# Kernel optimization log

Hardware: AMD Instinct MI355X
Metric: run time of the kernel (lower is better)

## Reference

```python
import jax, jax.numpy as jnp
import numpy as np

B, K, L, D, H, A = 32, 512, 6, 2048, 16, 10
HD = D // H
OBS = 128
MAX_STEPS = 512


def _ln(x, g, b, eps=1e-5):
    m = x.mean(-1, keepdims=True)
    v = ((x - m) ** 2).mean(-1, keepdims=True)
    return (x - m) * jax.lax.rsqrt(v + eps) * g + b


def _pos_encoding(seq_len, dim):
    # torch: seq counts down from seq_len-1 to 0
    seq = jnp.arange(seq_len - 1, -1, -1, dtype=jnp.float32)
    inv = 10000.0 ** (-(jnp.arange(0, dim, 2, dtype=jnp.float32)) / dim)
    si = seq[:, None] * inv[None, :]
    return jnp.concatenate([jnp.sin(si), jnp.cos(si)], axis=-1)  # [seq_len, dim]


def setup_inputs() -> dict:
    key = jax.random.key(0)
    ks = jax.random.split(key, 16)
    s = 0.02
    inp = {}
    inp['x'] = jax.random.normal(ks[0], (B, OBS), jnp.float32)
    inp['memories'] = jax.random.normal(ks[1], (B, K, L, D), jnp.float32)
    inp['mask'] = jax.random.randint(ks[2], (B, K), 0, 2, jnp.int32)
    inp['memory_indices'] = jax.random.randint(ks[3], (B, K), 0, MAX_STEPS, jnp.int32)
    # encoder (vector-obs Linear)
    inp['enc_w'] = jax.random.normal(ks[4], (D, OBS), jnp.float32) * s
    inp['enc_b'] = jnp.zeros((D,), jnp.float32)
    # per-layer params, stacked on leading L axis
    inp['lnq_g'] = jnp.ones((L, D), jnp.float32)
    inp['lnq_b'] = jnp.zeros((L, D), jnp.float32)
    inp['lnkv_g'] = jnp.ones((L, D), jnp.float32)
    inp['lnkv_b'] = jnp.zeros((L, D), jnp.float32)
    inp['lnattn_g'] = jnp.ones((L, D), jnp.float32)
    inp['lnattn_b'] = jnp.zeros((L, D), jnp.float32)
    inp['wq'] = jax.random.normal(ks[5], (L, HD, HD), jnp.float32) * s
    inp['wk'] = jax.random.normal(ks[6], (L, HD, HD), jnp.float32) * s
    inp['wv'] = jax.random.normal(ks[7], (L, HD, HD), jnp.float32) * s
    inp['wo'] = jax.random.normal(ks[8], (L, D, D), jnp.float32) * s
    inp['bo'] = jnp.zeros((L, D), jnp.float32)
    inp['fc_w'] = jax.random.normal(ks[9], (L, D, D), jnp.float32) * s
    inp['fc_b'] = jnp.zeros((L, D), jnp.float32)
    # heads
    inp['post_w'] = jax.random.normal(ks[10], (D, D), jnp.float32) * s
    inp['post_b'] = jnp.zeros((D,), jnp.float32)
    inp['actor_w'] = jax.random.normal(ks[11], (A, D), jnp.float32) * 0.01
    inp['actor_b'] = jnp.zeros((A,), jnp.float32)
    inp['critic_w'] = jax.random.normal(ks[12], (1, D), jnp.float32) * s
    inp['critic_b'] = jnp.zeros((1,), jnp.float32)
    return inp


def reference(x, memories, mask, memory_indices, enc_w, enc_b,
              lnq_g, lnq_b, lnkv_g, lnkv_b, lnattn_g, lnattn_b,
              wq, wk, wv, wo, bo, fc_w, fc_b,
              post_w, post_b, actor_w, actor_b, critic_w, critic_b):
    h = x @ enc_w.T + enc_b                              # [B, D] encoder
    pe = _pos_encoding(MAX_STEPS, D)[memory_indices]      # [B, K, D]
    mems = memories + pe[:, :, None, :]                   # [B, K, L, D]
    mems_t = jnp.moveaxis(mems, 2, 0)                     # [L, B, K, D]
    maskf = mask[:, None, :] != 0                         # [B, 1, K] -> bcast over heads
    inv_scale = 1.0 / jnp.sqrt(jnp.float32(D))            # note: full embed_dim, as in source

    def body(xq, p):
        lg, lb, kg, kb, ag, ab, Wq, Wk, Wv, Wo, bo_, Fw, Fb, mem = p
        q_ = _ln(xq, lg, lb)                              # [B, D] (query LN)
        kv = _ln(mem, kg, kb)                             # [B, K, D] (key = value = LN(mem))
        q = jnp.einsum('bhd,ed->bhe', q_.reshape(B, H, HD), Wq)
        k = jnp.einsum('bkhd,ed->bkhe', kv.reshape(B, K, H, HD), Wk)
        v = jnp.einsum('bkhd,ed->bkhe', kv.reshape(B, K, H, HD), Wv)
        energy = jnp.einsum('bhd,bkhd->bhk', q, k)        # [B, H, K]
        energy = jnp.where(maskf, energy, jnp.float32(-1e20))
        attn = jax.nn.softmax(energy * inv_scale, axis=-1)
        o = jnp.einsum('bhk,bkhd->bhd', attn, v).reshape(B, D)
        o = o @ Wo.T + bo_                                # fc_out
        xr = o + xq                                       # residual
        f = jax.nn.relu(_ln(xr, ag, ab) @ Fw.T + Fb)      # LN + MLP
        return f + xr, None

    h, _ = jax.lax.scan(
        body, h,
        (lnq_g, lnq_b, lnkv_g, lnkv_b, lnattn_g, lnattn_b,
         wq, wk, wv, wo, bo, fc_w, fc_b, mems_t))

    hid = jax.nn.relu(h @ post_w.T + post_b)
    logits = hid @ actor_w.T + actor_b                    # [B, A]
    value = hid @ critic_w.T + critic_b                   # [B, 1]
    return jnp.concatenate([logits, value], axis=-1)      # [B, A+1]
```

## Files before the change

### kernel.cpp

```cpp
#include <hip/hip_runtime.h>
#include <math.h>

namespace {

constexpr int B_ = 32, K_ = 512, L_ = 6, D_ = 2048, H_ = 16, HD_ = 128;
constexpr int OBS_ = 128, MAXS_ = 512, A_ = 10;
constexpr int NCH = 32, KC = K_ / NCH;
constexpr float EPS = 1e-5f;
constexpr float INV_SCALE = 0.022097086912079608f;

__device__ __forceinline__ float wsum64(float v) {
  v += __shfl_xor(v, 32); v += __shfl_xor(v, 16); v += __shfl_xor(v, 8);
  v += __shfl_xor(v, 4);  v += __shfl_xor(v, 2);  v += __shfl_xor(v, 1);
  return v;
}

__global__ __launch_bounds__(256) void k_pe(float* __restrict__ pe) {
  int s = blockIdx.x, t = threadIdx.x;
  float seqv = (float)(MAXS_ - 1 - s);
  const float c = 13.287712379549449f / 1024.0f;
  for (int r = 0; r < 8; ++r) {
    int j = t + 256 * r;
    int i = (j < 1024) ? j : j - 1024;
    float inv = exp2f(-c * (float)i);
    float a = seqv * inv;
    pe[(size_t)s * D_ + j] = (j < 1024) ? sinf(a) : cosf(a);
  }
}

__global__ __launch_bounds__(128) void k_enc(const float* __restrict__ x,
                                             const float* __restrict__ ew,
                                             const float* __restrict__ eb,
                                             float* __restrict__ h) {
  int b = blockIdx.x, et = blockIdx.y, t = threadIdx.x;
  __shared__ float xs[OBS_];
  xs[t] = x[b * OBS_ + t];
  __syncthreads();
  int e = et * 128 + t;
  const float* wr = ew + (size_t)e * OBS_;
  float acc = eb[e];
  for (int o = 0; o < OBS_; ++o) acc += xs[o] * wr[o];
  h[(size_t)b * D_ + e] = acc;
}

__global__ __launch_bounds__(256) void k_qw(const float* __restrict__ h,
                                            const float* __restrict__ g,
                                            const float* __restrict__ bvec,
                                            const float* __restrict__ Wq,
                                            const float* __restrict__ Wk,
                                            float* __restrict__ qW) {
  int b = blockIdx.x, t = threadIdx.x;
  int lane = t & 63, wv = t >> 6;
  __shared__ float qn[D_];
  __shared__ float qs[D_];
  __shared__ float rs[4], rq[4];
  float4 v0 = *(const float4*)(h + (size_t)b * D_ + t * 8);
  float4 v1 = *(const float4*)(h + (size_t)b * D_ + t * 8 + 4);
  float ls = v0.x + v0.y + v0.z + v0.w + v1.x + v1.y + v1.z + v1.w;
  float lq = v0.x * v0.x + v0.y * v0.y + v0.z * v0.z + v0.w * v0.w +
             v1.x * v1.x + v1.y * v1.y + v1.z * v1.z + v1.w * v1.w;
  ls = wsum64(ls); lq = wsum64(lq);
  if (lane == 0) { rs[wv] = ls; rq[wv] = lq; }
  __syncthreads();
  float sum = rs[0] + rs[1] + rs[2] + rs[3];
  float sq  = rq[0] + rq[1] + rq[2] + rq[3];
  float mean = sum * (1.f / D_);
  float rstd = rsqrtf(sq * (1.f / D_) - mean * mean + EPS);
  {
    float4 g0 = *(const float4*)(g + t * 8);
    float4 g1 = *(const float4*)(g + t * 8 + 4);
    float4 b0 = *(const float4*)(bvec + t * 8);
    float4 b1 = *(const float4*)(bvec + t * 8 + 4);
    qn[t * 8 + 0] = (v0.x - mean) * rstd * g0.x + b0.x;
    qn[t * 8 + 1] = (v0.y - mean) * rstd * g0.y + b0.y;
    qn[t * 8 + 2] = (v0.z - mean) * rstd * g0.z + b0.z;
    qn[t * 8 + 3] = (v0.w - mean) * rstd * g0.w + b0.w;
    qn[t * 8 + 4] = (v1.x - mean) * rstd * g1.x + b1.x;
    qn[t * 8 + 5] = (v1.y - mean) * rstd * g1.y + b1.y;
    qn[t * 8 + 6] = (v1.z - mean) * rstd * g1.z + b1.z;
    qn[t * 8 + 7] = (v1.w - mean) * rstd * g1.w + b1.w;
  }
  __syncthreads();
  int qid = t >> 4;
  int li = t & 15;
  for (int it = 0; it < 128; ++it) {
    int e = it;
    const float4* wr = (const float4*)(Wq + (size_t)e * HD_ + li * 8);
    const float4* qv = (const float4*)(qn + qid * HD_ + li * 8);
    float4 w0 = wr[0], w1 = wr[1], a0 = qv[0], a1 = qv[1];
    float acc = w0.x * a0.x + w0.y * a0.y + w0.z * a0.z + w0.w * a0.w +
                w1.x * a1.x + w1.y * a1.y + w1.z * a1.z + w1.w * a1.w;
    acc += __shfl_xor(acc, 1); acc += __shfl_xor(acc, 2);
    acc += __shfl_xor(acc, 4); acc += __shfl_xor(acc, 8);
    if (li == 0) qs[qid * HD_ + e] = acc;
  }
  __syncthreads();
  for (int r = 0; r < 8; ++r) {
    int j = t + 256 * r;
    int hh = j >> 7, d = j & 127;
    const float* qv = qs + hh * HD_;
    float acc = 0.f;
    for (int e = 0; e < HD_; ++e) acc += qv[e] * Wk[(size_t)e * HD_ + d];
    qW[(size_t)b * D_ + j] = acc * INV_SCALE;
  }
}

__global__ __launch_bounds__(512) void k_attn(const float* __restrict__ mem,
                                              const float* __restrict__ pe,
                                              const int* __restrict__ mask,
                                              const int* __restrict__ midx,
                                              const float* __restrict__ g,
                                              const float* __restrict__ bvec,
                                              const float* __restrict__ qW,
                                              float* __restrict__ pm,
                                              float* __restrict__ ps,
                                              float* __restrict__ pctx,
                                              int layer) {
  int b = blockIdx.x, ch = blockIdx.y;
  int t = threadIdx.x;
  int lane = t & 63, wv = t >> 6;
  int hh = t >> 5;
  int li = t & 31;
  __shared__ float redS[2][8], redQ[2][8];

  float4 g4 = *(const float4*)(g + t * 4);
  float4 b4 = *(const float4*)(bvec + t * 4);
  float4 qw4 = *(const float4*)(qW + (size_t)b * D_ + t * 4);

  float mrun = -INFINITY, srun = 0.f;
  float4 ctx = {0.f, 0.f, 0.f, 0.f};
  int it = 0;
  const size_t browbase = ((size_t)b * K_) * (L_ * D_) + (size_t)layer * D_;

  for (int kk = ch * KC; kk < ch * KC + KC; ++kk) {
    if (mask[b * K_ + kk] == 0) continue;
    int pidx = midx[b * K_ + kk];
    float4 xm = *(const float4*)(mem + browbase + (size_t)kk * (L_ * D_) + t * 4);
    float4 xp = *(const float4*)(pe + (size_t)pidx * D_ + t * 4);
    float4 x = {xm.x + xp.x, xm.y + xp.y, xm.z + xp.z, xm.w + xp.w};
    float lsv = x.x + x.y + x.z + x.w;
    float lqv = x.x * x.x + x.y * x.y + x.z * x.z + x.w * x.w;
    lsv = wsum64(lsv); lqv = wsum64(lqv);
    int p = it & 1;
    if (lane == 0) { redS[p][wv] = lsv; redQ[p][wv] = lqv; }
    __syncthreads();
    float sum = 0.f, sq = 0.f;
    #pragma unroll
    for (int w = 0; w < 8; ++w) { sum += redS[p][w]; sq += redQ[p][w]; }
    float mean = sum * (1.f / D_);
    float rstd = rsqrtf(sq * (1.f / D_) - mean * mean + EPS);
    float4 kv;
    kv.x = (x.x - mean) * rstd * g4.x + b4.x;
    kv.y = (x.y - mean) * rstd * g4.y + b4.y;
    kv.z = (x.z - mean) * rstd * g4.z + b4.z;
    kv.w = (x.w - mean) * rstd * g4.w + b4.w;
    float e = kv.x * qw4.x + kv.y * qw4.y + kv.z * qw4.z + kv.w * qw4.w;
    e += __shfl_xor(e, 1); e += __shfl_xor(e, 2); e += __shfl_xor(e, 4);
    e += __shfl_xor(e, 8); e += __shfl_xor(e, 16);
    float mnew = fmaxf(mrun, e);
    float sc = __expf(mrun - mnew);
    float w = __expf(e - mnew);
    srun = srun * sc + w;
    ctx.x = ctx.x * sc + w * kv.x;
    ctx.y = ctx.y * sc + w * kv.y;
    ctx.z = ctx.z * sc + w * kv.z;
    ctx.w = ctx.w * sc + w * kv.w;
    mrun = mnew;
    ++it;
  }
  size_t base = (size_t)(b * H_ + hh) * NCH + ch;
  *(float4*)(pctx + base * HD_ + 4 * li) = ctx;
  if (li == 0) { pm[base] = mrun; ps[base] = srun; }
}

__global__ __launch_bounds__(128) void k_reduce(const float* __restrict__ pm,
                                                const float* __restrict__ ps,
                                                const float* __restrict__ pctx,
                                                const float* __restrict__ Wv,
                                                float* __restrict__ opre) {
  int hh = blockIdx.x, b = blockIdx.y;
  int t = threadIdx.x;
  size_t base = (size_t)(b * H_ + hh) * NCH;
  float m = -INFINITY;
  for (int c = 0; c < NCH; ++c) m = fmaxf(m, pm[base + c]);
  float stot = 0.f, acc = 0.f;
  for (int c = 0; c < NCH; ++c) {
    float wc = __expf(pm[base + c] - m);
    stot += ps[base + c] * wc;
    acc += pctx[(base + c) * HD_ + t] * wc;
  }
  float ctxn = (stot > 0.f) ? acc / stot : 0.f;
  __shared__ float cs[HD_];
  cs[t] = ctxn;
  __syncthreads();
  const float* wr = Wv + (size_t)t * HD_;
  float o = 0.f;
  for (int d = 0; d < HD_; ++d) o += wr[d] * cs[d];
  opre[(size_t)b * D_ + hh * HD_ + t] = o;
}

__global__ __launch_bounds__(256) void k_wo(const float* __restrict__ opre,
                                            const float* __restrict__ Wo,
                                            const float* __restrict__ bo,
                                            const float* __restrict__ h,
                                            float* __restrict__ xr) {
  int b = blockIdx.x, et = blockIdx.y;
  int t = threadIdx.x, lane = t & 63, wv = t >> 6;
  __shared__ float xs[D_];
  for (int i = t; i < D_ / 4; i += 256)
    ((float4*)xs)[i] = ((const float4*)(opre + (size_t)b * D_))[i];
  __syncthreads();
  for (int j = 0; j < 16; ++j) {
    int e = et * 64 + wv * 16 + j;
    const float4* wr = (const float4*)(Wo + (size_t)e * D_);
    float acc = 0.f;
    for (int i = lane; i < D_ / 4; i += 64) {
      float4 w = wr[i]; float4 xv = ((float4*)xs)[i];
      acc += w.x * xv.x + w.y * xv.y + w.z * xv.z + w.w * xv.w;
    }
    acc = wsum64(acc);
    if (lane == 0) xr[(size_t)b * D_ + e] = acc + bo[e] + h[(size_t)b * D_ + e];
  }
}

__global__ __launch_bounds__(256) void k_fc(const float* __restrict__ xr,
                                            const float* __restrict__ g,
                                            const float* __restrict__ bvec,
                                            const float* __restrict__ Fw,
                                            const float* __restrict__ Fb,
                                            float* __restrict__ hout) {
  int b = blockIdx.x, et = blockIdx.y;
  int t = threadIdx.x, lane = t & 63, wv = t >> 6;
  __shared__ float raw[D_];
  __shared__ float nrm[D_];
  __shared__ float rs[4], rq[4];
  float ls = 0.f, lq = 0.f;
  for (int i = t; i < D_ / 4; i += 256) {
    float4 v = ((const float4*)(xr + (size_t)b * D_))[i];
    ((float4*)raw)[i] = v;
    ls += v.x + v.y + v.z + v.w;
    lq += v.x * v.x + v.y * v.y + v.z * v.z + v.w * v.w;
  }
  ls = wsum64(ls); lq = wsum64(lq);
  if (lane == 0) { rs[wv] = ls; rq[wv] = lq; }
  __syncthreads();
  float sum = rs[0] + rs[1] + rs[2] + rs[3];
  float sq  = rq[0] + rq[1] + rq[2] + rq[3];
  float mean = sum * (1.f / D_);
  float rstd = rsqrtf(sq * (1.f / D_) - mean * mean + EPS);
  for (int i = t; i < D_ / 4; i += 256) {
    float4 v = ((float4*)raw)[i];
    float4 g4 = ((const float4*)g)[i];
    float4 b4 = ((const float4*)bvec)[i];
    float4 n;
    n.x = (v.x - mean) * rstd * g4.x + b4.x;
    n.y = (v.y - mean) * rstd * g4.y + b4.y;
    n.z = (v.z - mean) * rstd * g4.z + b4.z;
    n.w = (v.w - mean) * rstd * g4.w + b4.w;
    ((float4*)nrm)[i] = n;
  }
  __syncthreads();
  for (int j = 0; j < 16; ++j) {
    int e = et * 64 + wv * 16 + j;
    const float4* wr = (const float4*)(Fw + (size_t)e * D_);
    float acc = 0.f;
    for (int i = lane; i < D_ / 4; i += 64) {
      float4 w = wr[i]; float4 xv = ((float4*)nrm)[i];
      acc += w.x * xv.x + w.y * xv.y + w.z * xv.z + w.w * xv.w;
    }
    acc = wsum64(acc);
    if (lane == 0)
      hout[(size_t)b * D_ + e] = fmaxf(acc + Fb[e], 0.f) + raw[e];
  }
}

__global__ __launch_bounds__(256) void k_post(const float* __restrict__ h,
                                              const float* __restrict__ Pw,
                                              const float* __restrict__ Pb,
                                              float* __restrict__ hid) {
  int b = blockIdx.x, et = blockIdx.y;
  int t = threadIdx.x, lane = t & 63, wv = t >> 6;
  __shared__ float xs[D_];
  for (int i = t; i < D_ / 4; i += 256)
    ((float4*)xs)[i] = ((const float4*)(h + (size_t)b * D_))[i];
  __syncthreads();
  for (int j = 0; j < 16; ++j) {
    int e = et * 64 + wv * 16 + j;
    const float4* wr = (const float4*)(Pw + (size_t)e * D_);
    float acc = 0.f;
    for (int i = lane; i < D_ / 4; i += 64) {
      float4 w = wr[i]; float4 xv = ((float4*)xs)[i];
      acc += w.x * xv.x + w.y * xv.y + w.z * xv.z + w.w * xv.w;
    }
    acc = wsum64(acc);
    if (lane == 0) hid[(size_t)b * D_ + e] = fmaxf(acc + Pb[e], 0.f);
  }
}

__global__ __launch_bounds__(256) void k_heads(const float* __restrict__ hid,
                                               const float* __restrict__ aw,
                                               const float* __restrict__ ab,
                                               const float* __restrict__ cw,
                                               const float* __restrict__ cb,
                                               float* __restrict__ out) {
  int b = blockIdx.x, j = blockIdx.y;
  int t = threadIdx.x, lane = t & 63, wv = t >> 6;
  const float* wr = (j < A_) ? (aw + (size_t)j * D_) : cw;
  float acc = 0.f;
  for (int i = t; i < D_ / 4; i += 256) {
    float4 w = ((const float4*)wr)[i];
    float4 xv = ((const float4*)(hid + (size_t)b * D_))[i];
    acc += w.x * xv.x + w.y * xv.y + w.z * xv.z + w.w * xv.w;
  }
  acc = wsum64(acc);
  __shared__ float r[4];
  if (lane == 0) r[wv] = acc;
  __syncthreads();
  if (t == 0) {
    float s = r[0] + r[1] + r[2] + r[3] + ((j < A_) ? ab[j] : cb[0]);
    out[b * (A_ + 1) + j] = s;
  }
}

}

extern "C" void kernel_launch(void* const* d_in, const int* in_sizes, int n_in,
                              void* d_out, int out_size, void* d_ws, size_t ws_size,
                              hipStream_t stream) {
  (void)in_sizes; (void)n_in; (void)out_size; (void)ws_size;
  const float* x      = (const float*)d_in[0];
  const float* mem    = (const float*)d_in[1];
  const int*   mask   = (const int*)d_in[2];
  const int*   midx   = (const int*)d_in[3];
  const float* enc_w  = (const float*)d_in[4];
  const float* enc_b  = (const float*)d_in[5];
  const float* lnq_g  = (const float*)d_in[6];
  const float* lnq_b  = (const float*)d_in[7];
  const float* lnkv_g = (const float*)d_in[8];
  const float* lnkv_b = (const float*)d_in[9];
  const float* lnat_g = (const float*)d_in[10];
  const float* lnat_b = (const float*)d_in[11];
  const float* wq     = (const float*)d_in[12];
  const float* wk     = (const float*)d_in[13];
  const float* wv     = (const float*)d_in[14];
  const float* wo     = (const float*)d_in[15];
  const float* bo     = (const float*)d_in[16];
  const float* fc_w   = (const float*)d_in[17];
  const float* fc_b   = (const float*)d_in[18];
  const float* post_w = (const float*)d_in[19];
  const float* post_b = (const float*)d_in[20];
  const float* act_w  = (const float*)d_in[21];
  const float* act_b  = (const float*)d_in[22];
  const float* cri_w  = (const float*)d_in[23];
  const float* cri_b  = (const float*)d_in[24];
  float* out = (float*)d_out;

  float* ws = (float*)d_ws;
  size_t off = 0;
  float* pe   = ws + off; off += (size_t)MAXS_ * D_;
  float* h    = ws + off; off += (size_t)B_ * D_;
  float* qW   = ws + off; off += (size_t)B_ * D_;
  float* opre = ws + off; off += (size_t)B_ * D_;
  float* xr   = ws + off; off += (size_t)B_ * D_;
  float* pm   = ws + off; off += (size_t)B_ * H_ * NCH;
  float* ps   = ws + off; off += (size_t)B_ * H_ * NCH;
  float* pctx = ws + off; off += (size_t)B_ * H_ * NCH * HD_;
  float* hid  = ws + off; off += (size_t)B_ * D_;

  hipLaunchKernelGGL(k_pe, dim3(MAXS_), dim3(256), 0, stream, pe);
  hipLaunchKernelGGL(k_enc, dim3(B_, D_ / 128), dim3(128), 0, stream, x, enc_w, enc_b, h);

  for (int l = 0; l < L_; ++l) {
    const float* Wq = wq + (size_t)l * HD_ * HD_;
    const float* Wk = wk + (size_t)l * HD_ * HD_;
    const float* Wv = wv + (size_t)l * HD_ * HD_;
    const float* Wo = wo + (size_t)l * D_ * D_;
    const float* Fw = fc_w + (size_t)l * D_ * D_;
    hipLaunchKernelGGL(k_qw, dim3(B_), dim3(256), 0, stream,
                       h, lnq_g + (size_t)l * D_, lnq_b + (size_t)l * D_, Wq, Wk, qW);
    hipLaunchKernelGGL(k_attn, dim3(B_, NCH), dim3(512), 0, stream,
                       mem, pe, mask, midx,
                       lnkv_g + (size_t)l * D_, lnkv_b + (size_t)l * D_,
                       qW, pm, ps, pctx, l);
    hipLaunchKernelGGL(k_reduce, dim3(H_, B_), dim3(128), 0, stream,
                       pm, ps, pctx, Wv, opre);
    hipLaunchKernelGGL(k_wo, dim3(B_, D_ / 64), dim3(256), 0, stream,
                       opre, Wo, bo + (size_t)l * D_, h, xr);
    hipLaunchKernelGGL(k_fc, dim3(B_, D_ / 64), dim3(256), 0, stream,
                       xr, lnat_g + (size_t)l * D_, lnat_b + (size_t)l * D_,
                       Fw, fc_b + (size_t)l * D_, h);
  }

  hipLaunchKernelGGL(k_post, dim3(B_, D_ / 64), dim3(256), 0, stream, h, post_w, post_b, hid);
  hipLaunchKernelGGL(k_heads, dim3(B_, A_ + 1), dim3(256), 0, stream,
                     hid, act_w, act_b, cri_w, cri_b, out);
}
```

Measured before the change: 1.146 ms.

## Batch the dense layers over all rows with split-K, and give attention one wave per key chunk

The old dense kernels ran one block per batch row, so each D×D weight matrix was streamed from memory 32 times. The new k_mv kernel handles all 32 batch rows per weight tile, staging the inputs in shared memory and splitting the K dimension 8 ways; separate reduce kernels then add bias and residual and apply LayerNorm or ReLU. The attention kernel now gives each wavefront its own 8-key chunk and covers all 16 heads per lane. This removes the block-wide syncthreads that ran for every key, at the cost of more registers and more partial results to merge.

```diff
diff --git a/kernel.cpp b/kernel.cpp
--- a/kernel.cpp
+++ b/kernel.cpp
@@ -5,7 +5,8 @@
 
 constexpr int B_ = 32, K_ = 512, L_ = 6, D_ = 2048, H_ = 16, HD_ = 128;
 constexpr int OBS_ = 128, MAXS_ = 512, A_ = 10;
-constexpr int NCH = 32, KC = K_ / NCH;
+constexpr int NCH = 64, WKEYS = 8;
+constexpr int KSPLIT = 8, KCHUNK = 256;
 constexpr float EPS = 1e-5f;
 constexpr float INV_SCALE = 0.022097086912079608f;
 
@@ -83,8 +84,7 @@
   __syncthreads();
   int qid = t >> 4;
   int li = t & 15;
-  for (int it = 0; it < 128; ++it) {
-    int e = it;
+  for (int e = 0; e < 128; ++e) {
     const float4* wr = (const float4*)(Wq + (size_t)e * HD_ + li * 8);
     const float4* qv = (const float4*)(qn + qid * HD_ + li * 8);
     float4 w0 = wr[0], w1 = wr[1], a0 = qv[0], a1 = qv[1];
@@ -105,7 +105,7 @@
   }
 }
 
-__global__ __launch_bounds__(512) void k_attn(const float* __restrict__ mem,
+__global__ __launch_bounds__(256) void k_attn(const float* __restrict__ mem,
                                               const float* __restrict__ pe,
                                               const int* __restrict__ mask,
                                               const int* __restrict__ midx,
@@ -116,61 +116,84 @@
                                               float* __restrict__ ps,
                                               float* __restrict__ pctx,
                                               int layer) {
-  int b = blockIdx.x, ch = blockIdx.y;
+  int b = blockIdx.x;
   int t = threadIdx.x;
-  int lane = t & 63, wv = t >> 6;
-  int hh = t >> 5;
-  int li = t & 31;
-  __shared__ float redS[2][8], redQ[2][8];
-
-  float4 g4 = *(const float4*)(g + t * 4);
-  float4 b4 = *(const float4*)(bvec + t * 4);
-  float4 qw4 = *(const float4*)(qW + (size_t)b * D_ + t * 4);
-
-  float mrun = -INFINITY, srun = 0.f;
-  float4 ctx = {0.f, 0.f, 0.f, 0.f};
-  int it = 0;
+  int wid = t >> 6, l = t & 63;
+  int ch = blockIdx.y * 4 + wid;
+  int hi = l >> 5;
+  int ll = l & 31;
+
+  __shared__ float gs[D_], bs[D_], qs[D_];
+  for (int i = t; i < D_ / 4; i += 256) {
+    ((float4*)gs)[i] = ((const float4*)g)[i];
+    ((float4*)bs)[i] = ((const float4*)bvec)[i];
+    ((float4*)qs)[i] = ((const float4*)(qW + (size_t)b * D_))[i];
+  }
+  __syncthreads();
+
+  float m[8], s[8];
+  float4 ctx[8];
+  #pragma unroll
+  for (int i = 0; i < 8; ++i) {
+    m[i] = -INFINITY; s[i] = 0.f; ctx[i] = {0.f, 0.f, 0.f, 0.f};
+  }
+
   const size_t browbase = ((size_t)b * K_) * (L_ * D_) + (size_t)layer * D_;
-
-  for (int kk = ch * KC; kk < ch * KC + KC; ++kk) {
+  int kk0 = ch * WKEYS;
+  for (int kk = kk0; kk < kk0 + WKEYS; ++kk) {
     if (mask[b * K_ + kk] == 0) continue;
     int pidx = midx[b * K_ + kk];
-    float4 xm = *(const float4*)(mem + browbase + (size_t)kk * (L_ * D_) + t * 4);
-    float4 xp = *(const float4*)(pe + (size_t)pidx * D_ + t * 4);
-    float4 x = {xm.x + xp.x, xm.y + xp.y, xm.z + xp.z, xm.w + xp.w};
-    float lsv = x.x + x.y + x.z + x.w;
-    float lqv = x.x * x.x + x.y * x.y + x.z * x.z + x.w * x.w;
-    lsv = wsum64(lsv); lqv = wsum64(lqv);
-    int p = it & 1;
-    if (lane == 0) { redS[p][wv] = lsv; redQ[p][wv] = lqv; }
-    __syncthreads();
-    float sum = 0.f, sq = 0.f;
+    const float4* mp = (const float4*)(mem + browbase + (size_t)kk * (L_ * D_));
+    const float4* pp = (const float4*)(pe + (size_t)pidx * D_);
+    float4 x[8];
     #pragma unroll
-    for (int w = 0; w < 8; ++w) { sum += redS[p][w]; sq += redQ[p][w]; }
-    float mean = sum * (1.f / D_);
-    float rstd = rsqrtf(sq * (1.f / D_) - mean * mean + EPS);
-    float4 kv;
-    kv.x = (x.x - mean) * rstd * g4.x + b4.x;
-    kv.y = (x.y - mean) * rstd * g4.y + b4.y;
-    kv.z = (x.z - mean) * rstd * g4.z + b4.z;
-    kv.w = (x.w - mean) * rstd * g4.w + b4.w;
-    float e = kv.x * qw4.x + kv.y * qw4.y + kv.z * qw4.z + kv.w * qw4.w;
-    e += __shfl_xor(e, 1); e += __shfl_xor(e, 2); e += __shfl_xor(e, 4);
-    e += __shfl_xor(e, 8); e += __shfl_xor(e, 16);
-    float mnew = fmaxf(mrun, e);
-    float sc = __expf(mrun - mnew);
-    float w = __expf(e - mnew);
-    srun = srun * sc + w;
-    ctx.x = ctx.x * sc + w * kv.x;
-    ctx.y = ctx.y * sc + w * kv.y;
-    ctx.z = ctx.z * sc + w * kv.z;
-    ctx.w = ctx.w * sc + w * kv.w;
-    mrun = mnew;
-    ++it;
-  }
-  size_t base = (size_t)(b * H_ + hh) * NCH + ch;
-  *(float4*)(pctx + base * HD_ + 4 * li) = ctx;
-  if (li == 0) { pm[base] = mrun; ps[base] = srun; }
+    for (int i = 0; i < 8; ++i) {
+      float4 a = mp[i * 64 + l];
+      float4 c = pp[i * 64 + l];
+      x[i] = {a.x + c.x, a.y + c.y, a.z + c.z, a.w + c.w};
+    }
+    float ls = 0.f, lq = 0.f;
+    #pragma unroll
+    for (int i = 0; i < 8; ++i) {
+      ls += x[i].x + x[i].y + x[i].z + x[i].w;
+      lq += x[i].x * x[i].x + x[i].y * x[i].y + x[i].z * x[i].z + x[i].w * x[i].w;
+    }
+    ls = wsum64(ls); lq = wsum64(lq);
+    float mean = ls * (1.f / D_);
+    float rstd = rsqrtf(lq * (1.f / D_) - mean * mean + EPS);
+    #pragma unroll
+    for (int i = 0; i < 8; ++i) {
+      int idx = i * 64 + l;
+      float4 g4 = ((const float4*)gs)[idx];
+      float4 b4 = ((const float4*)bs)[idx];
+      float4 q4 = ((const float4*)qs)[idx];
+      float4 kv;
+      kv.x = (x[i].x - mean) * rstd * g4.x + b4.x;
+      kv.y = (x[i].y - mean) * rstd * g4.y + b4.y;
+      kv.z = (x[i].z - mean) * rstd * g4.z + b4.z;
+      kv.w = (x[i].w - mean) * rstd * g4.w + b4.w;
+      float p = kv.x * q4.x + kv.y * q4.y + kv.z * q4.z + kv.w * q4.w;
+      p += __shfl_xor(p, 1); p += __shfl_xor(p, 2); p += __shfl_xor(p, 4);
+      p += __shfl_xor(p, 8); p += __shfl_xor(p, 16);
+      float mn = fmaxf(m[i], p);
+      float sc = __expf(m[i] - mn);
+      float w = __expf(p - mn);
+      s[i] = s[i] * sc + w;
+      ctx[i].x = ctx[i].x * sc + w * kv.x;
+      ctx[i].y = ctx[i].y * sc + w * kv.y;
+      ctx[i].z = ctx[i].z * sc + w * kv.z;
+      ctx[i].w = ctx[i].w * sc + w * kv.w;
+      m[i] = mn;
+    }
+  }
+
+  #pragma unroll
+  for (int i = 0; i < 8; ++i) {
+    int head = 2 * i + hi;
+    size_t base = (size_t)(b * H_ + head) * NCH + ch;
+    *(float4*)(pctx + base * HD_ + 4 * ll) = ctx[i];
+    if (ll == 0) { pm[base] = m[i]; ps[base] = s[i]; }
+  }
 }
 
 __global__ __launch_bounds__(128) void k_reduce(const float* __restrict__ pm,
@@ -199,47 +222,63 @@
   opre[(size_t)b * D_ + hh * HD_ + t] = o;
 }
 
-__global__ __launch_bounds__(256) void k_wo(const float* __restrict__ opre,
-                                            const float* __restrict__ Wo,
-                                            const float* __restrict__ bo,
-                                            const float* __restrict__ h,
-                                            float* __restrict__ xr) {
-  int b = blockIdx.x, et = blockIdx.y;
-  int t = threadIdx.x, lane = t & 63, wv = t >> 6;
-  __shared__ float xs[D_];
-  for (int i = t; i < D_ / 4; i += 256)
-    ((float4*)xs)[i] = ((const float4*)(opre + (size_t)b * D_))[i];
-  __syncthreads();
-  for (int j = 0; j < 16; ++j) {
-    int e = et * 64 + wv * 16 + j;
-    const float4* wr = (const float4*)(Wo + (size_t)e * D_);
-    float acc = 0.f;
-    for (int i = lane; i < D_ / 4; i += 64) {
-      float4 w = wr[i]; float4 xv = ((float4*)xs)[i];
-      acc += w.x * xv.x + w.y * xv.y + w.z * xv.z + w.w * xv.w;
-    }
-    acc = wsum64(acc);
-    if (lane == 0) xr[(size_t)b * D_ + e] = acc + bo[e] + h[(size_t)b * D_ + e];
-  }
-}
-
-__global__ __launch_bounds__(256) void k_fc(const float* __restrict__ xr,
-                                            const float* __restrict__ g,
-                                            const float* __restrict__ bvec,
-                                            const float* __restrict__ Fw,
-                                            const float* __restrict__ Fb,
-                                            float* __restrict__ hout) {
-  int b = blockIdx.x, et = blockIdx.y;
-  int t = threadIdx.x, lane = t & 63, wv = t >> 6;
-  __shared__ float raw[D_];
-  __shared__ float nrm[D_];
+__global__ __launch_bounds__(256) void k_mv(const float* __restrict__ X,
+                                            const float* __restrict__ W,
+                                            float* __restrict__ part) {
+  int et = blockIdx.x, kc = blockIdx.y;
+  int t = threadIdx.x;
+  __shared__ float xs[32][260];
+  for (int r = 0; r < 8; ++r) {
+    int i = t + 256 * r;
+    int b = i >> 6, j = i & 63;
+    float4 v = *(const float4*)(X + (size_t)b * D_ + kc * KCHUNK + 4 * j);
+    *(float4*)(&xs[b][4 * j]) = v;
+  }
+  __syncthreads();
+  int b = t & 31, eg = t >> 5;
+  const float* wbase = W + (size_t)(et * 64 + eg * 8) * D_ + kc * KCHUNK;
+  float acc[8] = {0.f, 0.f, 0.f, 0.f, 0.f, 0.f, 0.f, 0.f};
+  for (int j = 0; j < 64; ++j) {
+    float4 x4 = *(const float4*)(&xs[b][4 * j]);
+    #pragma unroll
+    for (int i = 0; i < 8; ++i) {
+      float4 w4 = *(const float4*)(wbase + (size_t)i * D_ + 4 * j);
+      acc[i] += w4.x * x4.x + w4.y * x4.y + w4.z * x4.z + w4.w * x4.w;
+    }
+  }
+  float* pb = part + ((size_t)b * KSPLIT + kc) * D_ + et * 64 + eg * 8;
+  float4 o0 = {acc[0], acc[1], acc[2], acc[3]};
+  float4 o1 = {acc[4], acc[5], acc[6], acc[7]};
+  *(float4*)pb = o0;
+  *(float4*)(pb + 4) = o1;
+}
+
+__global__ __launch_bounds__(256) void k_mvred_ln(const float* __restrict__ part,
+                                                  const float* __restrict__ bias,
+                                                  const float* __restrict__ res,
+                                                  const float* __restrict__ g,
+                                                  const float* __restrict__ bvec,
+                                                  float* __restrict__ xr,
+                                                  float* __restrict__ xn) {
+  int b = blockIdx.x, t = threadIdx.x;
+  int lane = t & 63, wv = t >> 6;
   __shared__ float rs[4], rq[4];
+  float4 v[2];
   float ls = 0.f, lq = 0.f;
-  for (int i = t; i < D_ / 4; i += 256) {
-    float4 v = ((const float4*)(xr + (size_t)b * D_))[i];
-    ((float4*)raw)[i] = v;
-    ls += v.x + v.y + v.z + v.w;
-    lq += v.x * v.x + v.y * v.y + v.z * v.z + v.w * v.w;
+  #pragma unroll
+  for (int r = 0; r < 2; ++r) {
+    int e4 = t + 256 * r;
+    float4 a = {0.f, 0.f, 0.f, 0.f};
+    for (int kc = 0; kc < KSPLIT; ++kc) {
+      float4 p = ((const float4*)(part + ((size_t)b * KSPLIT + kc) * D_))[e4];
+      a.x += p.x; a.y += p.y; a.z += p.z; a.w += p.w;
+    }
+    float4 b4 = ((const float4*)bias)[e4];
+    float4 h4 = ((const float4*)(res + (size_t)b * D_))[e4];
+    a.x += b4.x + h4.x; a.y += b4.y + h4.y; a.z += b4.z + h4.z; a.w += b4.w + h4.w;
+    v[r] = a;
+    ls += a.x + a.y + a.z + a.w;
+    lq += a.x * a.x + a.y * a.y + a.z * a.z + a.w * a.w;
   }
   ls = wsum64(ls); lq = wsum64(lq);
   if (lane == 0) { rs[wv] = ls; rq[wv] = lq; }
@@ -248,52 +287,43 @@
   float sq  = rq[0] + rq[1] + rq[2] + rq[3];
   float mean = sum * (1.f / D_);
   float rstd = rsqrtf(sq * (1.f / D_) - mean * mean + EPS);
-  for (int i = t; i < D_ / 4; i += 256) {
-    float4 v = ((float4*)raw)[i];
-    float4 g4 = ((const float4*)g)[i];
-    float4 b4 = ((const float4*)bvec)[i];
+  #pragma unroll
+  for (int r = 0; r < 2; ++r) {
+    int e4 = t + 256 * r;
+    float4 a = v[r];
+    ((float4*)(xr + (size_t)b * D_))[e4] = a;
+    float4 g4 = ((const float4*)g)[e4];
+    float4 b4 = ((const float4*)bvec)[e4];
     float4 n;
-    n.x = (v.x - mean) * rstd * g4.x + b4.x;
-    n.y = (v.y - mean) * rstd * g4.y + b4.y;
-    n.z = (v.z - mean) * rstd * g4.z + b4.z;
-    n.w = (v.w - mean) * rstd * g4.w + b4.w;
-    ((float4*)nrm)[i] = n;
-  }
-  __syncthreads();
-  for (int j = 0; j < 16; ++j) {
-    int e = et * 64 + wv * 16 + j;
-    const float4* wr = (const float4*)(Fw + (size_t)e * D_);
-    float acc = 0.f;
-    for (int i = lane; i < D_ / 4; i += 64) {
-      float4 w = wr[i]; float4 xv = ((float4*)nrm)[i];
-      acc += w.x * xv.x + w.y * xv.y + w.z * xv.z + w.w * xv.w;
-    }
-    acc = wsum64(acc);
-    if (lane == 0)
-      hout[(size_t)b * D_ + e] = fmaxf(acc + Fb[e], 0.f) + raw[e];
-  }
-}
-
-__global__ __launch_bounds__(256) void k_post(const float* __restrict__ h,
-                                              const float* __restrict__ Pw,
-                                              const float* __restrict__ Pb,
-                                              float* __restrict__ hid) {
-  int b = blockIdx.x, et = blockIdx.y;
-  int t = threadIdx.x, lane = t & 63, wv = t >> 6;
-  __shared__ float xs[D_];
-  for (int i = t; i < D_ / 4; i += 256)
-    ((float4*)xs)[i] = ((const float4*)(h + (size_t)b * D_))[i];
-  __syncthreads();
-  for (int j = 0; j < 16; ++j) {
-    int e = et * 64 + wv * 16 + j;
-    const float4* wr = (const float4*)(Pw + (size_t)e * D_);
-    float acc = 0.f;
-    for (int i = lane; i < D_ / 4; i += 64) {
-      float4 w = wr[i]; float4 xv = ((float4*)xs)[i];
-      acc += w.x * xv.x + w.y * xv.y + w.z * xv.z + w.w * xv.w;
-    }
-    acc = wsum64(acc);
-    if (lane == 0) hid[(size_t)b * D_ + e] = fmaxf(acc + Pb[e], 0.f);
+    n.x = (a.x - mean) * rstd * g4.x + b4.x;
+    n.y = (a.y - mean) * rstd * g4.y + b4.y;
+    n.z = (a.z - mean) * rstd * g4.z + b4.z;
+    n.w = (a.w - mean) * rstd * g4.w + b4.w;
+    ((float4*)(xn + (size_t)b * D_))[e4] = n;
+  }
+}
+
+__global__ __launch_bounds__(256) void k_mvred_relu(const float* __restrict__ part,
+                                                    const float* __restrict__ bias,
+                                                    const float* __restrict__ res,
+                                                    float* __restrict__ out) {
+  int b = blockIdx.x, t = threadIdx.x;
+  #pragma unroll
+  for (int r = 0; r < 2; ++r) {
+    int e4 = t + 256 * r;
+    float4 a = {0.f, 0.f, 0.f, 0.f};
+    for (int kc = 0; kc < KSPLIT; ++kc) {
+      float4 p = ((const float4*)(part + ((size_t)b * KSPLIT + kc) * D_))[e4];
+      a.x += p.x; a.y += p.y; a.z += p.z; a.w += p.w;
+    }
+    float4 b4 = ((const float4*)bias)[e4];
+    a.x = fmaxf(a.x + b4.x, 0.f); a.y = fmaxf(a.y + b4.y, 0.f);
+    a.z = fmaxf(a.z + b4.z, 0.f); a.w = fmaxf(a.w + b4.w, 0.f);
+    if (res) {
+      float4 h4 = ((const float4*)(res + (size_t)b * D_))[e4];
+      a.x += h4.x; a.y += h4.y; a.z += h4.z; a.w += h4.w;
+    }
+    ((float4*)(out + (size_t)b * D_))[e4] = a;
   }
 }
 
@@ -362,10 +392,12 @@
   float* qW   = ws + off; off += (size_t)B_ * D_;
   float* opre = ws + off; off += (size_t)B_ * D_;
   float* xr   = ws + off; off += (size_t)B_ * D_;
+  float* xn   = ws + off; off += (size_t)B_ * D_;
+  float* hid  = ws + off; off += (size_t)B_ * D_;
   float* pm   = ws + off; off += (size_t)B_ * H_ * NCH;
   float* ps   = ws + off; off += (size_t)B_ * H_ * NCH;
   float* pctx = ws + off; off += (size_t)B_ * H_ * NCH * HD_;
-  float* hid  = ws + off; off += (size_t)B_ * D_;
+  float* part = ws + off; off += (size_t)B_ * KSPLIT * D_;
 
   hipLaunchKernelGGL(k_pe, dim3(MAXS_), dim3(256), 0, stream, pe);
   hipLaunchKernelGGL(k_enc, dim3(B_, D_ / 128), dim3(128), 0, stream, x, enc_w, enc_b, h);
@@ -378,20 +410,24 @@
     const float* Fw = fc_w + (size_t)l * D_ * D_;
     hipLaunchKernelGGL(k_qw, dim3(B_), dim3(256), 0, stream,
                        h, lnq_g + (size_t)l * D_, lnq_b + (size_t)l * D_, Wq, Wk, qW);
-    hipLaunchKernelGGL(k_attn, dim3(B_, NCH), dim3(512), 0, stream,
+    hipLaunchKernelGGL(k_attn, dim3(B_, NCH / 4), dim3(256), 0, stream,
                        mem, pe, mask, midx,
                        lnkv_g + (size_t)l * D_, lnkv_b + (size_t)l * D_,
                        qW, pm, ps, pctx, l);
     hipLaunchKernelGGL(k_reduce, dim3(H_, B_), dim3(128), 0, stream,
                        pm, ps, pctx, Wv, opre);
-    hipLaunchKernelGGL(k_wo, dim3(B_, D_ / 64), dim3(256), 0, stream,
-                       opre, Wo, bo + (size_t)l * D_, h, xr);
-    hipLaunchKernelGGL(k_fc, dim3(B_, D_ / 64), dim3(256), 0, stream,
-                       xr, lnat_g + (size_t)l * D_, lnat_b + (size_t)l * D_,
-                       Fw, fc_b + (size_t)l * D_, h);
-  }
-
-  hipLaunchKernelGGL(k_post, dim3(B_, D_ / 64), dim3(256), 0, stream, h, post_w, post_b, hid);
+    hipLaunchKernelGGL(k_mv, dim3(D_ / 64, KSPLIT), dim3(256), 0, stream, opre, Wo, part);
+    hipLaunchKernelGGL(k_mvred_ln, dim3(B_), dim3(256), 0, stream,
+                       part, bo + (size_t)l * D_, h,
+                       lnat_g + (size_t)l * D_, lnat_b + (size_t)l * D_, xr, xn);
+    hipLaunchKernelGGL(k_mv, dim3(D_ / 64, KSPLIT), dim3(256), 0, stream, xn, Fw, part);
+    hipLaunchKernelGGL(k_mvred_relu, dim3(B_), dim3(256), 0, stream,
+                       part, fc_b + (size_t)l * D_, xr, h);
+  }
+
+  hipLaunchKernelGGL(k_mv, dim3(D_ / 64, KSPLIT), dim3(256), 0, stream, h, post_w, part);
+  hipLaunchKernelGGL(k_mvred_relu, dim3(B_), dim3(256), 0, stream,
+                     part, post_b, (const float*)nullptr, hid);
   hipLaunchKernelGGL(k_heads, dim3(B_, A_ + 1), dim3(256), 0, stream,
                      hid, act_w, act_b, cri_w, cri_b, out);
 }
```

New measurement: 1.077 ms. -6.1%, faster.
